# Kernel optimization log

Hardware: AMD Instinct MI355X
Metric: run time of the kernel (lower is better)

The kernel has to match this reference:

```python
import jax, jax.numpy as jnp
import numpy as np

N, FIN, NH, NR, F, E = 50000, 256, 4, 4, 64, 500000


def setup_inputs() -> dict:
    key = jax.random.key(0)
    ks = jax.random.split(key, 12)
    x = jax.random.normal(ks[0], (N, FIN), jnp.float32)
    src = jax.random.randint(ks[1], (E,), 0, N)
    trg = jax.random.randint(ks[2], (E,), 0, N)
    rel = jax.random.randint(ks[3], (E,), 0, NR)
    node_to_graph_map = jnp.zeros((N,), jnp.int32)
    s = 1.0 / np.sqrt(FIN)
    W_proj = jax.random.uniform(ks[4], (NH * NR * F, FIN), jnp.float32, -s, s)
    score_src = jax.random.normal(ks[5], (1, NH, NR, F), jnp.float32) * 0.1
    score_trg = jax.random.normal(ks[6], (1, NH, NR, F), jnp.float32) * 0.1
    sf = 1.0 / np.sqrt(F)
    W1 = jax.random.uniform(ks[7], (F, F), jnp.float32, -sf, sf)
    b1 = jnp.zeros((F,), jnp.float32)
    W2 = jax.random.uniform(ks[8], (F, F), jnp.float32, -sf, sf)
    b2 = jnp.zeros((F,), jnp.float32)
    W3 = jax.random.uniform(ks[9], (1, F), jnp.float32, -sf, sf)
    b3 = jnp.zeros((1,), jnp.float32)
    W_skip = jax.random.uniform(ks[10], (NH * F, FIN), jnp.float32, -s, s)
    bias = jnp.zeros((NH * F,), jnp.float32)
    gamma = jnp.ones((NH * F,), jnp.float32)
    beta = jnp.zeros((NH * F,), jnp.float32)
    return dict(x=x, src=src, trg=trg, rel=rel, node_to_graph_map=node_to_graph_map,
                W_proj=W_proj, score_src=score_src, score_trg=score_trg,
                W1=W1, b1=b1, W2=W2, b2=b2, W3=W3, b3=b3,
                W_skip=W_skip, bias=bias, gamma=gamma, beta=beta)


def mish(v):
    return v * jnp.tanh(jax.nn.softplus(v))


def gat_forward(x, W_proj, score_src, score_trg, W1, b1, W2, b2, W3, b3,
                W_skip, bias, gamma, beta, src, trg, rel):
    n = x.shape[0]
    # (N, NH, NR, F) projected node features
    proj = (x @ W_proj.T).reshape(n, NH, NR, F)
    s_src = (proj * score_src).sum(-1)  # (N, NH, NR)
    s_trg = (proj * score_trg).sum(-1)  # (N, NH, NR)
    # lift to edges for their own relation: (E, NH)
    e_s = s_src[src, :, rel] + s_trg[trg, :, rel]
    e_s = jax.nn.leaky_relu(e_s, 0.2)
    # per-(relation, head) max over edges (matches per-relation max(dim=0) in the torch loop)
    m = jax.ops.segment_max(e_s, rel, num_segments=NR)  # (NR, NH)
    e_exp = jnp.exp(e_s - m[rel])
    # segment softmax grouped by (target node, relation)
    seg = trg * NR + rel
    denom = jax.ops.segment_sum(e_exp, seg, num_segments=n * NR)  # (N*NR, NH)
    att = e_exp / (denom[seg] + 1e-16)  # (E, NH)
    feat = proj[src, :, rel, :] * att[:, :, None]  # (E, NH, F)
    agg = jax.ops.segment_sum(feat, seg, num_segments=n * NR)  # (N*NR, NH, F)
    agg = agg.reshape(n, NR, NH, F).transpose(0, 2, 1, 3)  # (N, NH, NR, F)
    # AttentionedAggregationLayer: MLP score -> Mish -> softmax over relation dim -> weighted sum
    h = jax.nn.relu(agg @ W1.T + b1)
    h = jax.nn.relu(h @ W2.T + b2)
    sc = mish(h @ W3.T + b3)            # (N, NH, NR, 1)
    a_rel = jax.nn.softmax(sc, axis=-2)
    out = (agg * a_rel).sum(-2)          # (N, NH, F)
    # skip connection (FIN != NH*F per-head, so projected skip), concat heads, bias, ELU, LayerNorm
    out = out + (x @ W_skip.T).reshape(n, NH, F)
    out = out.reshape(n, NH * F) + bias
    out = jax.nn.elu(out)
    mu = out.mean(-1, keepdims=True)
    var = out.var(-1, keepdims=True)
    out = (out - mu) * jax.lax.rsqrt(var + 1e-5) * gamma + beta
    return out


def reference(x, src, trg, rel, node_to_graph_map, W_proj, score_src, score_trg,
              W1, b1, W2, b2, W3, b3, W_skip, bias, gamma, beta):
    return gat_forward(x, W_proj, score_src, score_trg, W1, b1, W2, b2, W3, b3,
                       W_skip, bias, gamma, beta, src, trg, rel)
```

## Files before the change

kernel.cpp:

```cpp
#include <hip/hip_runtime.h>

#define NNODES 50000
#define NEDGES 500000
#define NBINS  (NNODES * 4)
#define NSCANB 196
#define MPAD   50176

#define WF_W1    0
#define WF_B1    4096
#define WF_W2    4160
#define WF_B2    8256
#define WF_W3    8320
#define WF_B3    8384
#define WF_SSC   8388
#define WF_STC   9412
#define WF_BIAS  10436
#define WF_GAMMA 10692
#define WF_BETA  10948
#define WF_TOT   11204

typedef __attribute__((ext_vector_type(8))) short short8;
typedef __attribute__((ext_vector_type(4))) short short4v;
typedef __attribute__((ext_vector_type(4))) float floatx4;
typedef __attribute__((ext_vector_type(4))) unsigned int uint4v;

__device__ __forceinline__ float bf2f(unsigned short u) {
    return __uint_as_float(((unsigned)u) << 16);
}
__device__ __forceinline__ unsigned f2bf(float f) {
    unsigned u = __float_as_uint(f);
    u += 0x7fffu + ((u >> 16) & 1u);
    return u >> 16;
}
__device__ __forceinline__ int clampi(int v, int hi) { return v < 0 ? 0 : (v > hi ? hi : v); }

__device__ __forceinline__ short8 pack_bf16(const float* p) {
    short8 r;
#pragma unroll
    for (int j = 0; j < 8; j++) r[j] = (short)f2bf(p[j]);
    return r;
}

__global__ __launch_bounds__(256) void probe_k(const unsigned short* __restrict__ xs,
                                               unsigned* __restrict__ flag) {
    __shared__ unsigned cnt;
    if (threadIdx.x == 0) cnt = 0;
    __syncthreads();
    unsigned local = 0;
    for (int i = threadIdx.x; i < 8192; i += 256) {
        float v = bf2f(xs[i]);
        if (!(fabsf(v) < 1e10f)) local++;
    }
    atomicAdd(&cnt, local);
    __syncthreads();
    if (threadIdx.x == 0) *flag = (cnt > 256u) ? 1u : 0u;
}

__device__ __forceinline__ float ldf(const void* p, int i, bool f32) {
    return f32 ? ((const float*)p)[i] : bf2f(((const unsigned short*)p)[i]);
}

__global__ __launch_bounds__(1024) void wconv_k(const void* W1, const void* b1,
                                                const void* W2, const void* b2,
                                                const void* W3, const void* b3,
                                                const void* ssc, const void* stc,
                                                const void* bias, const void* gamma,
                                                const void* beta,
                                                const unsigned* __restrict__ flag,
                                                float* __restrict__ wf) {
    bool f32 = (*flag != 0u);
    for (int i = threadIdx.x; i < WF_TOT; i += 1024) {
        float v;
        if (i < WF_B1)          v = ldf(W1, i - WF_W1, f32);
        else if (i < WF_W2)     v = ldf(b1, i - WF_B1, f32);
        else if (i < WF_B2)     v = ldf(W2, i - WF_W2, f32);
        else if (i < WF_W3)     v = ldf(b2, i - WF_B2, f32);
        else if (i < WF_B3)     v = ldf(W3, i - WF_W3, f32);
        else if (i < WF_SSC) {
            int j = i - WF_B3;
            v = (j < 1) ? ldf(b3, j, f32) : 0.f;
        }
        else if (i < WF_STC)    v = ldf(ssc, i - WF_SSC, f32);
        else if (i < WF_BIAS)   v = ldf(stc, i - WF_STC, f32);
        else if (i < WF_GAMMA)  v = ldf(bias, i - WF_BIAS, f32);
        else if (i < WF_BETA)   v = ldf(gamma, i - WF_GAMMA, f32);
        else                    v = ldf(beta, i - WF_BETA, f32);
        wf[i] = v;
    }
}

__global__ __launch_bounds__(256) void convbf_k(const void* __restrict__ src,
                                                unsigned short* __restrict__ dst,
                                                int nelem, int npad,
                                                const unsigned* __restrict__ flag) {
    int i8 = (blockIdx.x * 256 + threadIdx.x) * 8;
    if (i8 >= npad) return;
    short8 o;
    if (i8 < nelem) {
        if (*flag) {
            const float* pf = (const float*)src + i8;
            floatx4 a = *(const floatx4*)pf;
            floatx4 b = *(const floatx4*)(pf + 4);
            o[0] = (short)f2bf(a[0]); o[1] = (short)f2bf(a[1]);
            o[2] = (short)f2bf(a[2]); o[3] = (short)f2bf(a[3]);
            o[4] = (short)f2bf(b[0]); o[5] = (short)f2bf(b[1]);
            o[6] = (short)f2bf(b[2]); o[7] = (short)f2bf(b[3]);
        } else {
            o = *(const short8*)((const unsigned short*)src + i8);
        }
    } else {
#pragma unroll
        for (int j = 0; j < 8; j++) o[j] = 0;
    }
    *(short8*)(dst + i8) = o;
}

__global__ __launch_bounds__(64) void gemm_fused_k(const unsigned short* __restrict__ A,
                                                   const unsigned short* __restrict__ Bp,
                                                   const unsigned short* __restrict__ Bs,
                                                   unsigned short* __restrict__ proj,
                                                   unsigned short* __restrict__ out16,
                                                   float* __restrict__ out32,
                                                   const float* __restrict__ wf,
                                                   float* __restrict__ s_src,
                                                   float* __restrict__ s_trg,
                                                   const unsigned* __restrict__ flag) {
    const bool cf32 = (*flag != 0u);
    const int lane = threadIdx.x & 63;
    const int l15 = lane & 15, q = lane >> 4;
    const int m0 = blockIdx.x * 64;
    const int cg0 = blockIdx.y * 4;

    short8 af[4][8];
#pragma unroll
    for (int mt = 0; mt < 4; mt++)
#pragma unroll
        for (int ks = 0; ks < 8; ks++)
            af[mt][ks] = *(const short8*)(A + (size_t)(m0 + mt * 16 + l15) * 256 + ks * 32 + q * 8);

    if (cg0 < 16) {
#pragma unroll 1
        for (int cgi = 0; cgi < 4; cgi++) {
            const int cg = cg0 + cgi;
            floatx4 acc[4][4];
#pragma unroll
            for (int i = 0; i < 4; i++)
#pragma unroll
                for (int j = 0; j < 4; j++) acc[i][j] = (floatx4){0.f, 0.f, 0.f, 0.f};
#pragma unroll
            for (int ks = 0; ks < 8; ks++) {
                short8 bfr[4];
#pragma unroll
                for (int nt = 0; nt < 4; nt++)
                    bfr[nt] = *(const short8*)(Bp + (size_t)(cg * 64 + nt * 16 + l15) * 256 + ks * 32 + q * 8);
#pragma unroll
                for (int mt = 0; mt < 4; mt++)
#pragma unroll
                    for (int nt = 0; nt < 4; nt++)
                        acc[mt][nt] = __builtin_amdgcn_mfma_f32_16x16x32_bf16(bfr[nt], af[mt][ks],
                                                                             acc[mt][nt], 0, 0, 0);
            }
            const int h = cg >> 2, r = cg & 3;
            const int colbase = (r * 4 + h) * 64;
            const int cell = h * 4 + r;
            floatx4 sa4[4], sb4[4];
#pragma unroll
            for (int nt = 0; nt < 4; nt++) {
                sa4[nt] = *(const floatx4*)(wf + WF_SSC + cell * 64 + nt * 16 + q * 4);
                sb4[nt] = *(const floatx4*)(wf + WF_STC + cell * 64 + nt * 16 + q * 4);
            }
#pragma unroll
            for (int mt = 0; mt < 4; mt++) {
                const int row = m0 + mt * 16 + l15;
                float pa = 0.f, pb = 0.f;
#pragma unroll
                for (int nt = 0; nt < 4; nt++) {
                    short4v sv;
#pragma unroll
                    for (int rg = 0; rg < 4; rg++) {
                        float v = acc[mt][nt][rg];
                        unsigned short vb = (unsigned short)f2bf(v);
                        sv[rg] = (short)vb;
                        float vr = bf2f(vb);
                        pa = fmaf(vr, sa4[nt][rg], pa);
                        pb = fmaf(vr, sb4[nt][rg], pb);
                    }
                    if (row < NNODES)
                        __builtin_nontemporal_store(sv,
                            (short4v*)(proj + (size_t)row * 1024 + colbase + nt * 16 + q * 4));
                }
                pa += __shfl_xor(pa, 16);
                pa += __shfl_xor(pa, 32);
                pb += __shfl_xor(pb, 16);
                pb += __shfl_xor(pb, 32);
                if (q == 0 && row < NNODES) {
                    s_src[row * 16 + cell] = pa;
                    s_trg[row * 16 + cell] = pb;
                }
            }
        }
    } else {
#pragma unroll 1
        for (int cg = 0; cg < 4; cg++) {
            floatx4 acc[4][4];
#pragma unroll
            for (int i = 0; i < 4; i++)
#pragma unroll
                for (int j = 0; j < 4; j++) acc[i][j] = (floatx4){0.f, 0.f, 0.f, 0.f};
#pragma unroll
            for (int ks = 0; ks < 8; ks++) {
                short8 bfr[4];
#pragma unroll
                for (int nt = 0; nt < 4; nt++)
                    bfr[nt] = *(const short8*)(Bs + (size_t)(cg * 64 + nt * 16 + l15) * 256 + ks * 32 + q * 8);
#pragma unroll
                for (int mt = 0; mt < 4; mt++)
#pragma unroll
                    for (int nt = 0; nt < 4; nt++)
                        acc[mt][nt] = __builtin_amdgcn_mfma_f32_16x16x32_bf16(bfr[nt], af[mt][ks],
                                                                             acc[mt][nt], 0, 0, 0);
            }
#pragma unroll
            for (int mt = 0; mt < 4; mt++) {
                const int row = m0 + mt * 16 + l15;
                if (row >= NNODES) continue;
#pragma unroll
                for (int nt = 0; nt < 4; nt++) {
                    if (cf32) {
                        floatx4 o = acc[mt][nt];
                        __builtin_nontemporal_store(o,
                            (floatx4*)(out32 + (size_t)row * 256 + cg * 64 + nt * 16 + q * 4));
                    } else {
                        short4v sv;
#pragma unroll
                        for (int rg = 0; rg < 4; rg++)
                            sv[rg] = (short)f2bf(acc[mt][nt][rg]);
                        __builtin_nontemporal_store(sv,
                            (short4v*)(out16 + (size_t)row * 256 + cg * 64 + nt * 16 + q * 4));
                    }
                }
            }
        }
    }
}

__global__ __launch_bounds__(256) void count_k(const int* __restrict__ trg,
                                               const int* __restrict__ rel,
                                               unsigned* __restrict__ counts, int E) {
    int e = blockIdx.x * 256 + threadIdx.x;
    if (e >= E) return;
    int g = clampi(trg[e], NNODES - 1);
    int r = clampi(rel[e], 3);
    atomicAdd(&counts[g * 4 + r], 1u);
}

__global__ __launch_bounds__(256) void scan1_k(const unsigned* __restrict__ counts,
                                               unsigned* __restrict__ offsets,
                                               unsigned* __restrict__ bsum) {
    __shared__ unsigned ts[256];
    int t = threadIdx.x;
    int base = blockIdx.x * 1024 + t * 4;
    uint4v c = {0u, 0u, 0u, 0u};
    if (base + 3 < NBINS) c = *(const uint4v*)(counts + base);
    else {
#pragma unroll
        for (int j = 0; j < 4; j++) c[j] = (base + j < NBINS) ? counts[base + j] : 0u;
    }
    ts[t] = c[0] + c[1] + c[2] + c[3];
    __syncthreads();
    for (int off = 1; off < 256; off <<= 1) {
        unsigned v = (t >= off) ? ts[t - off] : 0u;
        __syncthreads();
        ts[t] += v;
        __syncthreads();
    }
    unsigned pre = (t == 0) ? 0u : ts[t - 1];
    uint4v o;
    o[0] = pre;
    o[1] = pre + c[0];
    o[2] = pre + c[0] + c[1];
    o[3] = pre + c[0] + c[1] + c[2];
    if (base + 3 < NBINS) *(uint4v*)(offsets + base) = o;
    else {
#pragma unroll
        for (int j = 0; j < 4; j++) if (base + j < NBINS) offsets[base + j] = o[j];
    }
    if (t == 255) bsum[blockIdx.x] = ts[255];
}

__global__ __launch_bounds__(256) void scan2_k(unsigned* __restrict__ bsum,
                                               unsigned* __restrict__ offsets) {
    __shared__ unsigned ts[256];
    int t = threadIdx.x;
    unsigned v = (t < NSCANB) ? bsum[t] : 0u;
    ts[t] = v;
    __syncthreads();
    for (int off = 1; off < 256; off <<= 1) {
        unsigned u = (t >= off) ? ts[t - off] : 0u;
        __syncthreads();
        ts[t] += u;
        __syncthreads();
    }
    if (t < NSCANB) bsum[t] = (t == 0) ? 0u : ts[t - 1];
    if (t == 255) offsets[NBINS] = ts[255];
}

__global__ __launch_bounds__(256) void scan3_k(unsigned* __restrict__ offsets,
                                               unsigned* __restrict__ cursor,
                                               const unsigned* __restrict__ bsum) {
    int t = threadIdx.x;
    unsigned base = bsum[blockIdx.x];
    int idx = blockIdx.x * 1024 + t * 4;
    if (idx + 3 < NBINS) {
        uint4v o = *(const uint4v*)(offsets + idx);
        o[0] += base; o[1] += base; o[2] += base; o[3] += base;
        *(uint4v*)(offsets + idx) = o;
        *(uint4v*)(cursor + idx) = o;
    } else {
#pragma unroll
        for (int j = 0; j < 4; j++)
            if (idx + j < NBINS) {
                unsigned v = offsets[idx + j] + base;
                offsets[idx + j] = v;
                cursor[idx + j] = v;
            }
    }
}

__global__ __launch_bounds__(256) void fill_k(const int* __restrict__ src,
                                              const int* __restrict__ trg,
                                              const int* __restrict__ rel,
                                              const float* __restrict__ s_src,
                                              const float* __restrict__ s_trg,
                                              unsigned* __restrict__ cursor,
                                              unsigned* __restrict__ esrc,
                                              floatx4* __restrict__ eexp, int E) {
    int e = blockIdx.x * 256 + threadIdx.x;
    if (e >= E) return;
    int s = clampi(src[e], NNODES - 1);
    int g = clampi(trg[e], NNODES - 1);
    int r = clampi(rel[e], 3);
    unsigned pos = atomicAdd(&cursor[g * 4 + r], 1u);
    if (pos >= (unsigned)E) pos = E - 1;
    esrc[pos] = (unsigned)s;
    floatx4 v;
#pragma unroll
    for (int h = 0; h < 4; h++) {
        float val = s_src[s * 16 + h * 4 + r] + s_trg[g * 16 + h * 4 + r];
        val = val > 0.f ? val : 0.2f * val;
        v[h] = expf(val);
    }
    eexp[pos] = v;
}

__global__ __launch_bounds__(256) void rowagg2_k(const unsigned* __restrict__ offsets,
                                                 const unsigned* __restrict__ esrc,
                                                 const floatx4* __restrict__ eexp,
                                                 const unsigned short* __restrict__ proj,
                                                 unsigned short* __restrict__ agg) {
    int wave = threadIdx.x >> 6, lane = threadIdx.x & 63;
    int bin = blockIdx.x * 4 + wave;
    if (bin >= NBINS) return;
    int r = bin & 3;
    int h = lane >> 4;
    unsigned beg = offsets[bin], end = offsets[bin + 1];

    float a0 = 0.f, a1 = 0.f, a2 = 0.f, a3 = 0.f, den = 0.f;
    for (unsigned i = beg; i < end; i++) {
        unsigned s = esrc[i];
        floatx4 pe = eexp[i];
        float p = pe[h];
        const short4v* pp = (const short4v*)(proj + (size_t)s * 1024 + r * 256) + lane;
        short4v v = *pp;
        den += p;
        a0 = fmaf(p, bf2f((unsigned short)v[0]), a0);
        a1 = fmaf(p, bf2f((unsigned short)v[1]), a1);
        a2 = fmaf(p, bf2f((unsigned short)v[2]), a2);
        a3 = fmaf(p, bf2f((unsigned short)v[3]), a3);
    }
    float inv = 1.f / (den + 1e-16f);
    short4v o;
    o[0] = (short)f2bf(a0 * inv);
    o[1] = (short)f2bf(a1 * inv);
    o[2] = (short)f2bf(a2 * inv);
    o[3] = (short)f2bf(a3 * inv);
    *((short4v*)(agg + (size_t)bin * 256) + lane) = o;
}

__global__ __launch_bounds__(256, 2) void mlp_mfma_k(const unsigned short* __restrict__ agg,
                                                     const float* __restrict__ wf,
                                                     float* __restrict__ sc) {
    __shared__ float lds[4][16 * 68];
    const int wave = threadIdx.x >> 6;
    const int lane = threadIdx.x & 63;
    const int l15 = lane & 15, q = lane >> 4;
    float* L = lds[wave];

    short8 w1f[2][4], w2f[2][4];
#pragma unroll
    for (int ks = 0; ks < 2; ks++)
#pragma unroll
        for (int nt = 0; nt < 4; nt++) {
            w1f[ks][nt] = pack_bf16(wf + WF_W1 + (nt * 16 + l15) * 64 + ks * 32 + q * 8);
            w2f[ks][nt] = pack_bf16(wf + WF_W2 + (nt * 16 + l15) * 64 + ks * 32 + q * 8);
        }
    float b1v[4], b2v[4], w3v[4];
#pragma unroll
    for (int nt = 0; nt < 4; nt++) {
        b1v[nt] = wf[WF_B1 + nt * 16 + l15];
        b2v[nt] = wf[WF_B2 + nt * 16 + l15];
        w3v[nt] = wf[WF_W3 + nt * 16 + l15];
    }
    float b3v = wf[WF_B3];

    int wave_id = blockIdx.x * 4 + wave;
#pragma unroll 1
    for (int t = 0; t < 4; t++) {
        int row0 = (wave_id * 4 + t) * 16;
        short8 a1[2];
#pragma unroll
        for (int ks = 0; ks < 2; ks++)
            a1[ks] = *(const short8*)(agg + (size_t)(row0 + l15) * 64 + ks * 32 + q * 8);
        floatx4 acc1[4];
#pragma unroll
        for (int nt = 0; nt < 4; nt++) {
            acc1[nt] = (floatx4){0.f, 0.f, 0.f, 0.f};
            acc1[nt] = __builtin_amdgcn_mfma_f32_16x16x32_bf16(a1[0], w1f[0][nt], acc1[nt], 0, 0, 0);
            acc1[nt] = __builtin_amdgcn_mfma_f32_16x16x32_bf16(a1[1], w1f[1][nt], acc1[nt], 0, 0, 0);
        }
        __syncthreads();
#pragma unroll
        for (int nt = 0; nt < 4; nt++)
#pragma unroll
            for (int rg = 0; rg < 4; rg++)
                L[(q * 4 + rg) * 68 + nt * 16 + l15] = fmaxf(acc1[nt][rg] + b1v[nt], 0.f);
        __syncthreads();
        short8 a2[2];
#pragma unroll
        for (int ks = 0; ks < 2; ks++) {
            short8 rr;
#pragma unroll
            for (int j = 0; j < 8; j++)
                rr[j] = (short)f2bf(L[l15 * 68 + ks * 32 + q * 8 + j]);
            a2[ks] = rr;
        }
        floatx4 acc2[4];
#pragma unroll
        for (int nt = 0; nt < 4; nt++) {
            acc2[nt] = (floatx4){0.f, 0.f, 0.f, 0.f};
            acc2[nt] = __builtin_amdgcn_mfma_f32_16x16x32_bf16(a2[0], w2f[0][nt], acc2[nt], 0, 0, 0);
            acc2[nt] = __builtin_amdgcn_mfma_f32_16x16x32_bf16(a2[1], w2f[1][nt], acc2[nt], 0, 0, 0);
        }
        float p[4];
#pragma unroll
        for (int rg = 0; rg < 4; rg++) {
            float s = 0.f;
#pragma unroll
            for (int nt = 0; nt < 4; nt++)
                s = fmaf(fmaxf(acc2[nt][rg] + b2v[nt], 0.f), w3v[nt], s);
            p[rg] = s;
        }
#pragma unroll
        for (int off = 1; off < 16; off <<= 1) {
#pragma unroll
            for (int rg = 0; rg < 4; rg++) p[rg] += __shfl_xor(p[rg], off);
        }
        if (l15 == 0) {
#pragma unroll
            for (int rg = 0; rg < 4; rg++) {
                float acc = p[rg] + b3v;
                float sp = fmaxf(acc, 0.f) + log1pf(expf(-fabsf(acc)));
                float m = acc * tanhf(sp);
                int s_id = row0 + q * 4 + rg;
                int n = s_id >> 4, r = (s_id >> 2) & 3, h = s_id & 3;
                sc[n * 16 + h * 4 + r] = m;
            }
        }
    }
}

__global__ __launch_bounds__(256) void final_k(const unsigned short* __restrict__ agg,
                                               const float* __restrict__ sc,
                                               const float* __restrict__ wf,
                                               const unsigned* __restrict__ flag,
                                               unsigned short* __restrict__ out16,
                                               float* __restrict__ out32) {
    const bool f32 = (*flag != 0u);
    int n = blockIdx.x, t = threadIdx.x;
    int h = t >> 6, f = t & 63;
    float s0 = sc[n * 16 + h * 4 + 0];
    float s1 = sc[n * 16 + h * 4 + 1];
    float s2 = sc[n * 16 + h * 4 + 2];
    float s3 = sc[n * 16 + h * 4 + 3];
    float mx = fmaxf(fmaxf(s0, s1), fmaxf(s2, s3));
    float e0 = expf(s0 - mx), e1 = expf(s1 - mx), e2 = expf(s2 - mx), e3 = expf(s3 - mx);
    float inv = 1.f / (e0 + e1 + e2 + e3);
    size_t base = (size_t)n * 1024 + h * 64 + f;
    float a0 = bf2f(agg[base]);
    float a1 = bf2f(agg[base + 256]);
    float a2 = bf2f(agg[base + 512]);
    float a3 = bf2f(agg[base + 768]);
    float v = (e0 * a0 + e1 * a1 + e2 * a2 + e3 * a3) * inv;
    size_t oidx = (size_t)n * 256 + t;
    float skipv = f32 ? out32[oidx] : bf2f(out16[oidx]);
    v += skipv + wf[WF_BIAS + t];
    v = v > 0.f ? v : expm1f(v);

    float s = v, qq = v * v;
#pragma unroll
    for (int o = 1; o < 64; o <<= 1) {
        s += __shfl_xor(s, o);
        qq += __shfl_xor(qq, o);
    }
    __shared__ float red[8];
    __shared__ float stat[2];
    int wv = t >> 6, ln = t & 63;
    if (ln == 0) { red[wv] = s; red[4 + wv] = qq; }
    __syncthreads();
    if (t == 0) {
        float S = red[0] + red[1] + red[2] + red[3];
        float Q = red[4] + red[5] + red[6] + red[7];
        float mu = S * (1.f / 256.f);
        float var = fmaxf(Q * (1.f / 256.f) - mu * mu, 0.f);
        stat[0] = mu;
        stat[1] = rsqrtf(var + 1e-5f);
    }
    __syncthreads();
    float o = (v - stat[0]) * stat[1] * wf[WF_GAMMA + t] + wf[WF_BETA + t];
    if (f32) out32[oidx] = o;
    else     out16[oidx] = (unsigned short)f2bf(o);
}

extern "C" void kernel_launch(void* const* d_in, const int* in_sizes, int n_in,
                              void* d_out, int out_size, void* d_ws, size_t ws_size,
                              hipStream_t stream) {
    if (ws_size < 226900000) return;

    const void* x      = d_in[0];
    const int* src     = (const int*)d_in[1];
    const int* trg     = (const int*)d_in[2];
    const int* rel     = (const int*)d_in[3];
    const void* W_proj = d_in[5];
    const void* ssc    = d_in[6];
    const void* stc    = d_in[7];
    const void* W1     = d_in[8];
    const void* b1     = d_in[9];
    const void* W2     = d_in[10];
    const void* b2     = d_in[11];
    const void* W3     = d_in[12];
    const void* b3     = d_in[13];
    const void* W_skip = d_in[14];
    const void* bias   = d_in[15];
    const void* gamma  = d_in[16];
    const void* beta   = d_in[17];
    unsigned short* out16 = (unsigned short*)d_out;
    float* out32          = (float*)d_out;

    char* w = (char*)d_ws;
    unsigned short* proj = (unsigned short*)(w + 0);
    unsigned short* agg  = (unsigned short*)(w + 102400000);
    unsigned short* xbf  = (unsigned short*)(w + 102400000);
    float* s_src         = (float*)(w + 204800000);
    float* s_trg         = (float*)(w + 208000000);
    floatx4* eexp        = (floatx4*)(w + 211200000);
    unsigned short* wpbf = (unsigned short*)(w + 211200000);
    unsigned short* wsbf = (unsigned short*)(w + 212300000);
    unsigned* esrc       = (unsigned*)(w + 219200000);
    unsigned* counts     = (unsigned*)(w + 221200000);
    unsigned* offsets    = (unsigned*)(w + 222000000);
    unsigned* cursor     = (unsigned*)(w + 222800016);
    float* sc            = (float*)(w + 223600016);
    float* wf            = (float*)(w + 226800016);
    unsigned* flag       = (unsigned*)(w + 226844840);
    unsigned* bsum       = (unsigned*)(w + 226844848);

    hipMemsetAsync(counts, 0, NBINS * 4, stream);

    probe_k<<<1, 256, 0, stream>>>((const unsigned short*)x, flag);
    wconv_k<<<1, 1024, 0, stream>>>(W1, b1, W2, b2, W3, b3, ssc, stc, bias, gamma, beta,
                                    flag, wf);
    convbf_k<<<(MPAD * 256) / (8 * 256), 256, 0, stream>>>(x, xbf, NNODES * 256,
                                                           MPAD * 256, flag);
    convbf_k<<<128, 256, 0, stream>>>(W_proj, wpbf, 1024 * 256, 1024 * 256, flag);
    convbf_k<<<32, 256, 0, stream>>>(W_skip, wsbf, 256 * 256, 256 * 256, flag);
    gemm_fused_k<<<dim3(784, 5), 64, 0, stream>>>(xbf, wpbf, wsbf, proj, out16, out32,
                                                  wf, s_src, s_trg, flag);
    count_k<<<1954, 256, 0, stream>>>(trg, rel, counts, NEDGES);
    scan1_k<<<NSCANB, 256, 0, stream>>>(counts, offsets, bsum);
    scan2_k<<<1, 256, 0, stream>>>(bsum, offsets);
    scan3_k<<<NSCANB, 256, 0, stream>>>(offsets, cursor, bsum);
    fill_k<<<1954, 256, 0, stream>>>(src, trg, rel, s_src, s_trg, cursor, esrc, eexp, NEDGES);
    rowagg2_k<<<NBINS / 4, 256, 0, stream>>>(offsets, esrc, eexp, proj, agg);
    mlp_mfma_k<<<3125, 256, 0, stream>>>(agg, wf, sc);
    final_k<<<NNODES, 256, 0, stream>>>(agg, sc, wf, flag, out16, out32);
}
```

Before: 630.9 us.

## Transpose score layout, drop nontemporal stores, unroll rowagg, wave-per-node final kernel

The score arrays s_src/s_trg are now written relation-major (r*4+h), so fill_k can read all four heads with one vector load instead of four scattered scalar loads. The GEMM epilogue switches from nontemporal to plain stores, likely so proj and the skip output stay in cache for later kernels. rowagg2_k unrolls its edge loop by two to keep more gathers in flight, and two __syncthreads are removed from the MLP kernel. final_k is rewritten so each wave handles one whole node with vectorized 4-element accesses and a wave-only LayerNorm reduction, removing shared memory and block barriers. Removing the MLP barriers may create a shared-memory race if waves share the L buffer.

Result: faster. 532.8 us (-15.6%).

```diff
diff --git a/kernel.cpp b/kernel.cpp
--- a/kernel.cpp
+++ b/kernel.cpp
@@ -162,12 +162,13 @@
             }
             const int h = cg >> 2, r = cg & 3;
             const int colbase = (r * 4 + h) * 64;
-            const int cell = h * 4 + r;
+            const int cell = r * 4 + h;
+            const int scell = h * 4 + r;
             floatx4 sa4[4], sb4[4];
 #pragma unroll
             for (int nt = 0; nt < 4; nt++) {
-                sa4[nt] = *(const floatx4*)(wf + WF_SSC + cell * 64 + nt * 16 + q * 4);
-                sb4[nt] = *(const floatx4*)(wf + WF_STC + cell * 64 + nt * 16 + q * 4);
+                sa4[nt] = *(const floatx4*)(wf + WF_SSC + scell * 64 + nt * 16 + q * 4);
+                sb4[nt] = *(const floatx4*)(wf + WF_STC + scell * 64 + nt * 16 + q * 4);
             }
 #pragma unroll
             for (int mt = 0; mt < 4; mt++) {
@@ -186,8 +187,7 @@
                         pb = fmaf(vr, sb4[nt][rg], pb);
                     }
                     if (row < NNODES)
-                        __builtin_nontemporal_store(sv,
-                            (short4v*)(proj + (size_t)row * 1024 + colbase + nt * 16 + q * 4));
+                        *(short4v*)(proj + (size_t)row * 1024 + colbase + nt * 16 + q * 4) = sv;
                 }
                 pa += __shfl_xor(pa, 16);
                 pa += __shfl_xor(pa, 32);
@@ -228,15 +228,13 @@
                 for (int nt = 0; nt < 4; nt++) {
                     if (cf32) {
                         floatx4 o = acc[mt][nt];
-                        __builtin_nontemporal_store(o,
-                            (floatx4*)(out32 + (size_t)row * 256 + cg * 64 + nt * 16 + q * 4));
+                        *(floatx4*)(out32 + (size_t)row * 256 + cg * 64 + nt * 16 + q * 4) = o;
                     } else {
                         short4v sv;
 #pragma unroll
                         for (int rg = 0; rg < 4; rg++)
                             sv[rg] = (short)f2bf(acc[mt][nt][rg]);
-                        __builtin_nontemporal_store(sv,
-                            (short4v*)(out16 + (size_t)row * 256 + cg * 64 + nt * 16 + q * 4));
+                        *(short4v*)(out16 + (size_t)row * 256 + cg * 64 + nt * 16 + q * 4) = sv;
                     }
                 }
             }
@@ -343,10 +341,12 @@
     unsigned pos = atomicAdd(&cursor[g * 4 + r], 1u);
     if (pos >= (unsigned)E) pos = E - 1;
     esrc[pos] = (unsigned)s;
+    floatx4 aa = *(const floatx4*)(s_src + s * 16 + r * 4);
+    floatx4 bb = *(const floatx4*)(s_trg + g * 16 + r * 4);
     floatx4 v;
 #pragma unroll
     for (int h = 0; h < 4; h++) {
-        float val = s_src[s * 16 + h * 4 + r] + s_trg[g * 16 + h * 4 + r];
+        float val = aa[h] + bb[h];
         val = val > 0.f ? val : 0.2f * val;
         v[h] = expf(val);
     }
@@ -366,17 +366,33 @@
     unsigned beg = offsets[bin], end = offsets[bin + 1];
 
     float a0 = 0.f, a1 = 0.f, a2 = 0.f, a3 = 0.f, den = 0.f;
-    for (unsigned i = beg; i < end; i++) {
-        unsigned s = esrc[i];
-        floatx4 pe = eexp[i];
-        float p = pe[h];
-        const short4v* pp = (const short4v*)(proj + (size_t)s * 1024 + r * 256) + lane;
-        short4v v = *pp;
-        den += p;
-        a0 = fmaf(p, bf2f((unsigned short)v[0]), a0);
-        a1 = fmaf(p, bf2f((unsigned short)v[1]), a1);
-        a2 = fmaf(p, bf2f((unsigned short)v[2]), a2);
-        a3 = fmaf(p, bf2f((unsigned short)v[3]), a3);
+    unsigned i = beg;
+    for (; i + 2 <= end; i += 2) {
+        unsigned s0 = esrc[i], s1 = esrc[i + 1];
+        floatx4 pe0 = eexp[i], pe1 = eexp[i + 1];
+        short4v v0 = *((const short4v*)(proj + (size_t)s0 * 1024 + r * 256) + lane);
+        short4v v1 = *((const short4v*)(proj + (size_t)s1 * 1024 + r * 256) + lane);
+        float p0 = pe0[h], p1 = pe1[h];
+        den += p0 + p1;
+        a0 = fmaf(p0, bf2f((unsigned short)v0[0]), a0);
+        a1 = fmaf(p0, bf2f((unsigned short)v0[1]), a1);
+        a2 = fmaf(p0, bf2f((unsigned short)v0[2]), a2);
+        a3 = fmaf(p0, bf2f((unsigned short)v0[3]), a3);
+        a0 = fmaf(p1, bf2f((unsigned short)v1[0]), a0);
+        a1 = fmaf(p1, bf2f((unsigned short)v1[1]), a1);
+        a2 = fmaf(p1, bf2f((unsigned short)v1[2]), a2);
+        a3 = fmaf(p1, bf2f((unsigned short)v1[3]), a3);
+    }
+    if (i < end) {
+        unsigned s0 = esrc[i];
+        floatx4 pe0 = eexp[i];
+        short4v v0 = *((const short4v*)(proj + (size_t)s0 * 1024 + r * 256) + lane);
+        float p0 = pe0[h];
+        den += p0;
+        a0 = fmaf(p0, bf2f((unsigned short)v0[0]), a0);
+        a1 = fmaf(p0, bf2f((unsigned short)v0[1]), a1);
+        a2 = fmaf(p0, bf2f((unsigned short)v0[2]), a2);
+        a3 = fmaf(p0, bf2f((unsigned short)v0[3]), a3);
     }
     float inv = 1.f / (den + 1e-16f);
     short4v o;
@@ -428,13 +444,11 @@
             acc1[nt] = __builtin_amdgcn_mfma_f32_16x16x32_bf16(a1[0], w1f[0][nt], acc1[nt], 0, 0, 0);
             acc1[nt] = __builtin_amdgcn_mfma_f32_16x16x32_bf16(a1[1], w1f[1][nt], acc1[nt], 0, 0, 0);
         }
-        __syncthreads();
 #pragma unroll
         for (int nt = 0; nt < 4; nt++)
 #pragma unroll
             for (int rg = 0; rg < 4; rg++)
                 L[(q * 4 + rg) * 68 + nt * 16 + l15] = fmaxf(acc1[nt][rg] + b1v[nt], 0.f);
-        __syncthreads();
         short8 a2[2];
 #pragma unroll
         for (int ks = 0; ks < 2; ks++) {
@@ -486,49 +500,68 @@
                                                unsigned short* __restrict__ out16,
                                                float* __restrict__ out32) {
     const bool f32 = (*flag != 0u);
-    int n = blockIdx.x, t = threadIdx.x;
-    int h = t >> 6, f = t & 63;
-    float s0 = sc[n * 16 + h * 4 + 0];
-    float s1 = sc[n * 16 + h * 4 + 1];
-    float s2 = sc[n * 16 + h * 4 + 2];
-    float s3 = sc[n * 16 + h * 4 + 3];
-    float mx = fmaxf(fmaxf(s0, s1), fmaxf(s2, s3));
-    float e0 = expf(s0 - mx), e1 = expf(s1 - mx), e2 = expf(s2 - mx), e3 = expf(s3 - mx);
+    const int wave = threadIdx.x >> 6, lane = threadIdx.x & 63;
+    const int n = blockIdx.x * 4 + wave;
+    const int h = lane >> 4;
+    const int c0 = h * 64 + (lane & 15) * 4;
+
+    floatx4 sv = *(const floatx4*)(sc + n * 16 + h * 4);
+    float mx = fmaxf(fmaxf(sv[0], sv[1]), fmaxf(sv[2], sv[3]));
+    float e0 = expf(sv[0] - mx), e1 = expf(sv[1] - mx);
+    float e2 = expf(sv[2] - mx), e3 = expf(sv[3] - mx);
     float inv = 1.f / (e0 + e1 + e2 + e3);
-    size_t base = (size_t)n * 1024 + h * 64 + f;
-    float a0 = bf2f(agg[base]);
-    float a1 = bf2f(agg[base + 256]);
-    float a2 = bf2f(agg[base + 512]);
-    float a3 = bf2f(agg[base + 768]);
-    float v = (e0 * a0 + e1 * a1 + e2 * a2 + e3 * a3) * inv;
-    size_t oidx = (size_t)n * 256 + t;
-    float skipv = f32 ? out32[oidx] : bf2f(out16[oidx]);
-    v += skipv + wf[WF_BIAS + t];
-    v = v > 0.f ? v : expm1f(v);
-
-    float s = v, qq = v * v;
+    float er[4] = {e0 * inv, e1 * inv, e2 * inv, e3 * inv};
+
+    float acc4[4] = {0.f, 0.f, 0.f, 0.f};
+#pragma unroll
+    for (int r = 0; r < 4; r++) {
+        short4v av = *(const short4v*)(agg + (size_t)n * 1024 + r * 256 + c0);
+        float e = er[r];
+        acc4[0] = fmaf(e, bf2f((unsigned short)av[0]), acc4[0]);
+        acc4[1] = fmaf(e, bf2f((unsigned short)av[1]), acc4[1]);
+        acc4[2] = fmaf(e, bf2f((unsigned short)av[2]), acc4[2]);
+        acc4[3] = fmaf(e, bf2f((unsigned short)av[3]), acc4[3]);
+    }
+
+    const size_t ob = (size_t)n * 256 + c0;
+    float v[4];
+    floatx4 bi = *(const floatx4*)(wf + WF_BIAS + c0);
+    if (f32) {
+        floatx4 sk = *(const floatx4*)(out32 + ob);
+#pragma unroll
+        for (int j = 0; j < 4; j++) v[j] = acc4[j] + sk[j] + bi[j];
+    } else {
+        short4v sk = *(const short4v*)(out16 + ob);
+#pragma unroll
+        for (int j = 0; j < 4; j++) v[j] = acc4[j] + bf2f((unsigned short)sk[j]) + bi[j];
+    }
+#pragma unroll
+    for (int j = 0; j < 4; j++) v[j] = v[j] > 0.f ? v[j] : expm1f(v[j]);
+
+    float s = v[0] + v[1] + v[2] + v[3];
+    float qq = v[0] * v[0] + v[1] * v[1] + v[2] * v[2] + v[3] * v[3];
 #pragma unroll
     for (int o = 1; o < 64; o <<= 1) {
         s += __shfl_xor(s, o);
         qq += __shfl_xor(qq, o);
     }
-    __shared__ float red[8];
-    __shared__ float stat[2];
-    int wv = t >> 6, ln = t & 63;
-    if (ln == 0) { red[wv] = s; red[4 + wv] = qq; }
-    __syncthreads();
-    if (t == 0) {
-        float S = red[0] + red[1] + red[2] + red[3];
-        float Q = red[4] + red[5] + red[6] + red[7];
-        float mu = S * (1.f / 256.f);
-        float var = fmaxf(Q * (1.f / 256.f) - mu * mu, 0.f);
-        stat[0] = mu;
-        stat[1] = rsqrtf(var + 1e-5f);
-    }
-    __syncthreads();
-    float o = (v - stat[0]) * stat[1] * wf[WF_GAMMA + t] + wf[WF_BETA + t];
-    if (f32) out32[oidx] = o;
-    else     out16[oidx] = (unsigned short)f2bf(o);
+    float mu = s * (1.f / 256.f);
+    float var = fmaxf(qq * (1.f / 256.f) - mu * mu, 0.f);
+    float rstd = rsqrtf(var + 1e-5f);
+
+    floatx4 ga = *(const floatx4*)(wf + WF_GAMMA + c0);
+    floatx4 be = *(const floatx4*)(wf + WF_BETA + c0);
+    if (f32) {
+        floatx4 o4;
+#pragma unroll
+        for (int j = 0; j < 4; j++) o4[j] = (v[j] - mu) * rstd * ga[j] + be[j];
+        *(floatx4*)(out32 + ob) = o4;
+    } else {
+        short4v o4;
+#pragma unroll
+        for (int j = 0; j < 4; j++) o4[j] = (short)f2bf((v[j] - mu) * rstd * ga[j] + be[j]);
+        *(short4v*)(out16 + ob) = o4;
+    }
 }
 
 extern "C" void kernel_launch(void* const* d_in, const int* in_sizes, int n_in,
@@ -592,5 +625,5 @@
     fill_k<<<1954, 256, 0, stream>>>(src, trg, rel, s_src, s_trg, cursor, esrc, eexp, NEDGES);
     rowagg2_k<<<NBINS / 4, 256, 0, stream>>>(offsets, esrc, eexp, proj, agg);
     mlp_mfma_k<<<3125, 256, 0, stream>>>(agg, wf, sc);
-    final_k<<<NNODES, 256, 0, stream>>>(agg, sc, wf, flag, out16, out32);
-}
+    final_k<<<12500, 256, 0, stream>>>(agg, sc, wf, flag, out16, out32);
+}
```
